# Kernel optimization log

Measured on AMD Instinct MI355X. Metric: run time of the kernel, lower is better.

The kernel has to match this reference:

```python
import jax, jax.numpy as jnp
import numpy as np

D_MODEL = 512
NHEAD = 8
HEAD_DIM = D_MODEL // NHEAD  # 64
ROTARY_DIM = HEAD_DIM        # rotary_dim defaults to head_dim
WINDOW = (127, 128)          # (left, right) sliding window, flash-attn convention
ROPE_BASE = 10000.0


def setup_inputs() -> dict:
    key = jax.random.key(0)
    k1, k2, k3, k4 = jax.random.split(key, 4)
    N, T = 4, 2048
    x = jax.random.normal(k1, (N, T, D_MODEL), dtype=jnp.float32)
    # Wqkv: Linear(d_model, 3*d_model, bias=False) -> weight [3*D, D]
    Wqkv_w = jax.random.normal(k2, (3 * D_MODEL, D_MODEL), dtype=jnp.float32) * (D_MODEL ** -0.5)
    # out_proj: Linear(d_model, d_model, bias=True)
    out_w = jax.random.normal(k3, (D_MODEL, D_MODEL), dtype=jnp.float32) * (D_MODEL ** -0.5)
    out_b = jax.random.normal(k4, (D_MODEL,), dtype=jnp.float32) * 0.01
    return {"x": x, "Wqkv_w": Wqkv_w, "out_w": out_w, "out_b": out_b}


def _rope_cos_sin(T, dtype):
    # flash-attn RotaryEmbedding: inv_freq over even indices of rotary_dim
    inv_freq = 1.0 / (ROPE_BASE ** (jnp.arange(0, ROTARY_DIM, 2, dtype=jnp.float32) / ROTARY_DIM))
    t = jnp.arange(T, dtype=jnp.float32)
    freqs = jnp.outer(t, inv_freq)  # [T, ROTARY_DIM//2]
    return jnp.cos(freqs).astype(dtype), jnp.sin(freqs).astype(dtype)


def _apply_rotary(x, cos, sin):
    # non-interleaved (rotate halves); x: [N, T, H, hd], rotary over first ROTARY_DIM dims
    r, rest = x[..., :ROTARY_DIM], x[..., ROTARY_DIM:]
    half = ROTARY_DIM // 2
    x1, x2 = r[..., :half], r[..., half:]
    c = cos[None, :, None, :]  # [1, T, 1, half]
    s = sin[None, :, None, :]
    rotated = jnp.concatenate([x1 * c - x2 * s, x2 * c + x1 * s], axis=-1)
    return jnp.concatenate([rotated, rest], axis=-1) if rest.shape[-1] else rotated


def reference(x, Wqkv_w, out_w, out_b):
    N, T, D = x.shape
    qkv = jnp.einsum('ntd,ed->nte', x, Wqkv_w).reshape(N, T, 3, NHEAD, HEAD_DIM)
    q, k, v = qkv[:, :, 0], qkv[:, :, 1], qkv[:, :, 2]  # each [N, T, H, hd]
    cos, sin = _rope_cos_sin(T, x.dtype)
    q = _apply_rotary(q, cos, sin)
    k = _apply_rotary(k, cos, sin)
    scale = HEAD_DIM ** -0.5
    scores = jnp.einsum('nthd,nshd->nhts', q, k) * scale  # [N, H, T, T]
    # sliding window: query i attends key j iff i - left <= j <= i + right
    i = jnp.arange(T)[:, None]
    j = jnp.arange(T)[None, :]
    mask = (j >= i - WINDOW[0]) & (j <= i + WINDOW[1])  # [T, T]
    scores = jnp.where(mask[None, None], scores, jnp.finfo(scores.dtype).min)
    attn = jax.nn.softmax(scores, axis=-1)
    ctx = jnp.einsum('nhts,nshd->nthd', attn, v).reshape(N, T, D)
    return jnp.einsum('ntd,ed->nte', ctx, out_w) + out_b
```

## Files before the change

kernel.cpp:

```cpp
#include <hip/hip_runtime.h>
#include <math.h>

#define TSEQ 2048
#define NB 4
#define DM 512
#define NH 8
#define HD 64

typedef _Float16 half8 __attribute__((ext_vector_type(8)));
typedef _Float16 half4 __attribute__((ext_vector_type(4)));
typedef float floatx4 __attribute__((ext_vector_type(4)));

#if __has_builtin(__builtin_amdgcn_exp2f)
#define EXP2F(x) __builtin_amdgcn_exp2f(x)
#else
#define EXP2F(x) exp2f(x)
#endif

__device__ __forceinline__ void gl2lds16(const _Float16* g, _Float16* l) {
  const __attribute__((address_space(1))) unsigned int* gp =
      (const __attribute__((address_space(1))) unsigned int*)(uintptr_t)g;
  __attribute__((address_space(3))) unsigned int* lp =
      (__attribute__((address_space(3))) unsigned int*)(uintptr_t)l;
  __builtin_amdgcn_global_load_lds(gp, lp, 16, 0, 0);
}


__device__ __forceinline__ void cvt8(const float* __restrict__ src, char* __restrict__ dst,
                                     int unit_src, int unit_dst) {
  const float4 a = ((const float4*)src)[2 * unit_src];
  const float4 b = ((const float4*)src)[2 * unit_src + 1];
  half8 h;
  h[0] = (_Float16)a.x; h[1] = (_Float16)a.y; h[2] = (_Float16)a.z; h[3] = (_Float16)a.w;
  h[4] = (_Float16)b.x; h[5] = (_Float16)b.y; h[6] = (_Float16)b.z; h[7] = (_Float16)b.w;
  *(half8*)(dst + (size_t)unit_dst * 16) = h;
}

__global__ void prep(const float* __restrict__ x, const float* __restrict__ wqkv,
                     const float* __restrict__ ow, char* __restrict__ ws) {
  const int i = blockIdx.x * 256 + threadIdx.x;
  if (i < 524288) {
    cvt8(x, ws, i, i);
  } else if (i < 622592) {
    const int o = i - 524288;
    cvt8(wqkv, ws + 8650752, o, o);
  } else if (i < 655360) {
    const int o = i - 622592;
    cvt8(ow, ws + 10485760, o, o);
  } else {
    const int u = i - 655360;
    float4 o4;
    {
      const int id = 2 * u, t = id >> 5, fi = id & 31;
      const float invf = powf(10000.0f, -(float)(2 * fi) * (1.0f / 64.0f));
      float s, c; sincosf((float)t * invf, &s, &c);
      o4.x = c; o4.y = s;
    }
    {
      const int id = 2 * u + 1, t = id >> 5, fi = id & 31;
      const float invf = powf(10000.0f, -(float)(2 * fi) * (1.0f / 64.0f));
      float s, c; sincosf((float)t * invf, &s, &c);
      o4.z = c; o4.w = s;
    }
    ((float4*)(ws + 46137344))[u] = o4;
  }
}

__global__ __launch_bounds__(256) void qkv_gemm_mfma(
    const _Float16* __restrict__ A, const _Float16* __restrict__ B,
    const float2* __restrict__ rope,
    _Float16* __restrict__ qb, _Float16* __restrict__ kb, _Float16* __restrict__ vT)
{
  __shared__ __align__(16) _Float16 As0[128 * 32];
  __shared__ __align__(16) _Float16 Bs0[128 * 32];
  __shared__ __align__(16) _Float16 As1[128 * 32];
  __shared__ __align__(16) _Float16 Bs1[128 * 32];
  const int tid = threadIdx.x;
  const int wv = tid >> 6, lane = tid & 63, quad = lane >> 4, col = lane & 15;
  const int wm = wv >> 1, we = wv & 1;
  const int m0 = blockIdx.x << 7, c0 = blockIdx.y << 7;
  const int r0 = tid >> 2, p0 = tid & 3;
  const int cA0 = (p0 - (r0 >> 1)) & 3;
  const int r1 = (tid + 256) >> 2, p1 = tid & 3;
  const int cA1 = (p1 - (r1 >> 1)) & 3;
  const _Float16* ga0 = &A[(size_t)(m0 + r0) * DM + cA0 * 8];
  const _Float16* ga1 = &A[(size_t)(m0 + r1) * DM + cA1 * 8];
  const _Float16* gb0 = &B[(size_t)(c0 + r0) * DM + cA0 * 8];
  const _Float16* gb1 = &B[(size_t)(c0 + r1) * DM + cA1 * 8];
  floatx4 acc[4][4] = {};

#define QKV_STAGE(AS, BS, K)                      \
  do {                                            \
    gl2lds16(ga0 + (K), &AS[tid * 8]);            \
    gl2lds16(ga1 + (K), &AS[(tid + 256) * 8]);    \
    gl2lds16(gb0 + (K), &BS[tid * 8]);            \
    gl2lds16(gb1 + (K), &BS[(tid + 256) * 8]);    \
  } while (0)

#define QKV_COMPUTE(AS, BS)                                                   \
  do {                                                                        \
    half8 af[4], bf[4];                                                       \
    _Pragma("unroll") for (int mt = 0; mt < 4; mt++) {                        \
      const int R = wm * 64 + mt * 16 + col;                                  \
      af[mt] = *(const half8*)&AS[R * 32 + (((quad + (R >> 1)) & 3) << 3)];   \
    }                                                                         \
    _Pragma("unroll") for (int et = 0; et < 4; et++) {                        \
      const int R = we * 64 + et * 16 + col;                                  \
      bf[et] = *(const half8*)&BS[R * 32 + (((quad + (R >> 1)) & 3) << 3)];   \
    }                                                                         \
    _Pragma("unroll") for (int mt = 0; mt < 4; mt++)                          \
      _Pragma("unroll") for (int et = 0; et < 4; et++)                        \
        acc[mt][et] =                                                         \
            __builtin_amdgcn_mfma_f32_16x16x32_f16(af[mt], bf[et], acc[mt][et], 0, 0, 0); \
  } while (0)

  QKV_STAGE(As0, Bs0, 0);
  for (int k0 = 0; k0 < DM; k0 += 64) {
    __syncthreads();
    QKV_STAGE(As1, Bs1, k0 + 32);
    QKV_COMPUTE(As0, Bs0);
    __syncthreads();
    if (k0 + 64 < DM) QKV_STAGE(As0, Bs0, k0 + 64);
    QKV_COMPUTE(As1, Bs1);
  }
#undef QKV_STAGE
#undef QKV_COMPUTE

  const int eidx = (c0 >> 6) + we;
  const int three = eidx >> 3, h = eidx & 7;
  const int mbase = m0 + wm * 64 + quad * 4;
  if (three == 2) {
#pragma unroll
    for (int mt = 0; mt < 4; mt++) {
      const int m = mbase + mt * 16;
      const int n = m >> 11, t = m & 2047;
#pragma unroll
      for (int et = 0; et < 4; et++) {
        const int dh = et * 16 + col;
        half4 hv;
#pragma unroll
        for (int r = 0; r < 4; r++) hv[r] = (_Float16)acc[mt][et][r];
        *(half4*)&vT[(size_t)(n * NH + h) * HD * TSEQ + (size_t)dh * TSEQ + t] = hv;
      }
    }
  } else {
    _Float16* dst = three ? kb : qb;
    const float scl = three ? 1.0f : 0.125f * 1.4426950408889634f;
#pragma unroll
    for (int mt = 0; mt < 4; mt++)
#pragma unroll
      for (int r = 0; r < 4; r++) {
        const int m = mbase + mt * 16 + r;
        const int n = m >> 11, t = m & 2047;
#pragma unroll
        for (int et = 0; et < 4; et++) {
          const int i = ((et & 1) << 4) + col;
          const float2 cs = rope[t * 32 + i];
          const float v = acc[mt][et][r];
          const float v2 = acc[mt][et ^ 2][r];
          const float o = (et < 2) ? (v * cs.x - v2 * cs.y) : (v * cs.x + v2 * cs.y);
          dst[((size_t)(n * NH + h) * TSEQ + t) * HD + et * 16 + col] = (_Float16)(o * scl);
        }
      }
  }
}

__global__ __launch_bounds__(512, 4) void attn_win_mfma(
    const _Float16* __restrict__ qb, const _Float16* __restrict__ kb,
    const _Float16* __restrict__ vT, _Float16* __restrict__ ctx)
{
  __shared__ __align__(16) char smem[55296];
  _Float16* Ks = (_Float16*)smem;
  _Float16* Vt = (_Float16*)(smem + 9216);
  _Float16* Ps = (_Float16*)(smem + 18432);
  _Float16* Osh = (_Float16*)(smem + 36864);

  const int tid = threadIdx.x;
  const int wv = tid >> 6;
  const int lane = tid & 63;
  const int quad = lane >> 4;
  const int col = lane & 15;
  const int lin = (blockIdx.y << 4) | blockIdx.x;
  const int sl  = ((lin & 7) << 6) | (lin >> 3);
  const int nh = sl >> 4;
  const int q0 = (sl & 15) << 7;
  const _Float16* qp = qb + (size_t)nh * TSEQ * HD;
  const _Float16* kp = kb + (size_t)nh * TSEQ * HD;
  const _Float16* vp = vT + (size_t)nh * HD * TSEQ;

  const int i_row = (wv << 4) + col;
  const int ig = q0 + i_row;
  const half8 qf0 = *(const half8*)&qp[(size_t)ig * HD + (quad << 3)];
  const half8 qf1 = *(const half8*)&qp[(size_t)ig * HD + 32 + (quad << 3)];

  float l_i = 0.0f;
  floatx4 accO[4] = {};

  const int kt0 = max(0, q0 - 127) >> 6;
  const int kt1 = min(TSEQ - 1, q0 + 255) >> 6;
  const int kr = tid >> 3, kc = (tid & 7) << 3;
  const _Float16* kpr = kp + (size_t)kr * HD + kc;
  const _Float16* vpr = vp + (size_t)kr * TSEQ + kc;
  const int iw0 = q0 + (wv << 4);

  half8 ck = *(const half8*)(kpr + (size_t)(kt0 << 6) * HD);
  half8 cv = *(const half8*)(vpr + (kt0 << 6));

  for (int kt = kt0; kt <= kt1; kt++) {
    const int j0 = kt << 6;
    __syncthreads();
    *(half8*)&Ks[kr * 72 + kc] = ck;
    *(half8*)&Vt[kr * 72 + kc] = cv;
    __syncthreads();

    {
      const int jn = (kt < kt1) ? (j0 + 64) : j0;
      ck = *(const half8*)(kpr + (size_t)jn * HD);
      cv = *(const half8*)(vpr + jn);
    }

    if ((unsigned)(j0 - iw0 + 190) >= 334u) continue;

    floatx4 S[4];
#pragma unroll
    for (int js = 0; js < 4; js++) {
      const int jlo = j0 + (js << 4);
      if ((unsigned)(jlo - iw0 + 142) < 286u) {
        const half8 a0 = *(const half8*)&Ks[((js << 4) + col) * 72 + (quad << 3)];
        const half8 a1 = *(const half8*)&Ks[((js << 4) + col) * 72 + 32 + (quad << 3)];
        floatx4 c = {0.f, 0.f, 0.f, 0.f};
        c = __builtin_amdgcn_mfma_f32_16x16x32_f16(a0, qf0, c, 0, 0, 0);
        c = __builtin_amdgcn_mfma_f32_16x16x32_f16(a1, qf1, c, 0, 0, 0);
        S[js] = c;
      }
    }
    const int relb = j0 - ig + 127 + (quad << 2);
#pragma unroll
    for (int js = 0; js < 4; js++) {
      const int jlo = j0 + (js << 4);
      if ((unsigned)(jlo - iw0 + 142) < 286u) {
        half4 ph;
#pragma unroll
        for (int r = 0; r < 4; r++) {
          const bool valid = (unsigned)(relb + (js << 4) + r) < 256u;
          const float p = valid ? EXP2F(S[js][r]) : 0.0f;
          l_i += p;
          ph[r] = (_Float16)p;
        }
        *(half4*)&Ps[i_row * 72 + (js << 4) + (quad << 2)] = ph;
      } else {
        const half4 zz = {(_Float16)0.f, (_Float16)0.f, (_Float16)0.f, (_Float16)0.f};
        *(half4*)&Ps[i_row * 72 + (js << 4) + (quad << 2)] = zz;
      }
    }
    const half8 pa0 = *(const half8*)&Ps[i_row * 72 + (quad << 3)];
    const half8 pa1 = *(const half8*)&Ps[i_row * 72 + 32 + (quad << 3)];
#pragma unroll
    for (int d4 = 0; d4 < 4; d4++) {
      const half8 vb0 = *(const half8*)&Vt[((d4 << 4) + col) * 72 + (quad << 3)];
      const half8 vb1 = *(const half8*)&Vt[((d4 << 4) + col) * 72 + 32 + (quad << 3)];
      accO[d4] = __builtin_amdgcn_mfma_f32_16x16x32_f16(pa0, vb0, accO[d4], 0, 0, 0);
      accO[d4] = __builtin_amdgcn_mfma_f32_16x16x32_f16(pa1, vb1, accO[d4], 0, 0, 0);
    }
  }
  l_i += __shfl_xor(l_i, 16, 64);
  l_i += __shfl_xor(l_i, 32, 64);
  {
    const float linv = 1.0f / l_i;
    float l4[4];
#pragma unroll
    for (int r = 0; r < 4; r++) l4[r] = __shfl(linv, (quad << 2) + r, 64);
#pragma unroll
    for (int d4 = 0; d4 < 4; d4++)
#pragma unroll
      for (int r = 0; r < 4; r++)
        Osh[((wv << 4) + (quad << 2) + r) * 72 + (d4 << 4) + col] = (_Float16)(accO[d4][r] * l4[r]);
  }
  __syncthreads();
  {
    const int n = nh >> 3, h = nh & 7;
    const int oi = tid >> 2, oc = (tid & 3) << 4;
    _Float16* dst = &ctx[((size_t)n * TSEQ + q0 + oi) * DM + h * HD + oc];
    *(half8*)&dst[0] = *(const half8*)&Osh[oi * 72 + oc];
    *(half8*)&dst[8] = *(const half8*)&Osh[oi * 72 + oc + 8];
  }
}

__global__ __launch_bounds__(256) void out_gemm_mfma(
    const _Float16* __restrict__ A, const _Float16* __restrict__ B,
    const float* __restrict__ bias, float* __restrict__ out)
{
  __shared__ __align__(16) _Float16 As0[128 * 32];
  __shared__ __align__(16) _Float16 Bs0[64 * 32];
  __shared__ __align__(16) _Float16 As1[128 * 32];
  __shared__ __align__(16) _Float16 Bs1[64 * 32];
  const int tid = threadIdx.x;
  const int wv = tid >> 6, lane = tid & 63, quad = lane >> 4, col = lane & 15;
  const int wm = wv >> 1, we = wv & 1;
  const int m0 = blockIdx.x << 7, c0 = blockIdx.y << 6;
  const int r0 = tid >> 2, p0 = tid & 3;
  const int cA0 = (p0 - (r0 >> 1)) & 3;
  const int r1 = (tid + 256) >> 2;
  const int cA1 = (p0 - (r1 >> 1)) & 3;
  const _Float16* ga0 = &A[(size_t)(m0 + r0) * DM + cA0 * 8];
  const _Float16* ga1 = &A[(size_t)(m0 + r1) * DM + cA1 * 8];
  const _Float16* gb0 = &B[(size_t)(c0 + r0) * DM + cA0 * 8];
  floatx4 acc[4][2] = {};

#define OG_STAGE(AS, BS, K)                       \
  do {                                            \
    gl2lds16(ga0 + (K), &AS[tid * 8]);            \
    gl2lds16(ga1 + (K), &AS[(tid + 256) * 8]);    \
    gl2lds16(gb0 + (K), &BS[tid * 8]);            \
  } while (0)

#define OG_COMPUTE(AS, BS)                                                    \
  do {                                                                        \
    half8 af[4], bf[2];                                                       \
    _Pragma("unroll") for (int mt = 0; mt < 4; mt++) {                        \
      const int R = wm * 64 + mt * 16 + col;                                  \
      af[mt] = *(const half8*)&AS[R * 32 + (((quad + (R >> 1)) & 3) << 3)];   \
    }                                                                         \
    _Pragma("unroll") for (int et = 0; et < 2; et++) {                        \
      const int R = we * 32 + et * 16 + col;                                  \
      bf[et] = *(const half8*)&BS[R * 32 + (((quad + (R >> 1)) & 3) << 3)];   \
    }                                                                         \
    _Pragma("unroll") for (int mt = 0; mt < 4; mt++)                          \
      _Pragma("unroll") for (int et = 0; et < 2; et++)                        \
        acc[mt][et] =                                                         \
            __builtin_amdgcn_mfma_f32_16x16x32_f16(af[mt], bf[et], acc[mt][et], 0, 0, 0); \
  } while (0)

  OG_STAGE(As0, Bs0, 0);
  for (int k0 = 0; k0 < DM; k0 += 64) {
    __syncthreads();
    OG_STAGE(As1, Bs1, k0 + 32);
    OG_COMPUTE(As0, Bs0);
    __syncthreads();
    if (k0 + 64 < DM) OG_STAGE(As0, Bs0, k0 + 64);
    OG_COMPUTE(As1, Bs1);
  }
#undef OG_STAGE
#undef OG_COMPUTE

  float bb[2];
#pragma unroll
  for (int et = 0; et < 2; et++) bb[et] = bias[c0 + we * 32 + et * 16 + col];
  const int mbase = m0 + wm * 64 + quad * 4;
#pragma unroll
  for (int mt = 0; mt < 4; mt++)
#pragma unroll
    for (int r = 0; r < 4; r++) {
      const int m = mbase + mt * 16 + r;
#pragma unroll
      for (int et = 0; et < 2; et++)
        out[(size_t)m * DM + c0 + we * 32 + et * 16 + col] = acc[mt][et][r] + bb[et];
    }
}

extern "C" void kernel_launch(void* const* d_in, const int* in_sizes, int n_in,
                              void* d_out, int out_size, void* d_ws, size_t ws_size,
                              hipStream_t stream) {
  const float* x    = (const float*)d_in[0];
  const float* wqkv = (const float*)d_in[1];
  const float* ow   = (const float*)d_in[2];
  const float* ob   = (const float*)d_in[3];
  char* ws = (char*)d_ws;
  _Float16* xh    = (_Float16*)(ws);
  _Float16* wqkvh = (_Float16*)(ws + 8650752);
  _Float16* owh   = (_Float16*)(ws + 10485760);
  _Float16* qbuf  = (_Float16*)(ws + 11534336);
  _Float16* kbuf  = (_Float16*)(ws + 20971520);
  _Float16* vTb   = (_Float16*)(ws + 29360128);
  _Float16* ctxh  = (_Float16*)(ws + 37748736);
  float2*   rope  = (float2*)  (ws + 46137344);

  prep<<<2688, 256, 0, stream>>>(x, wqkv, ow, ws);
  qkv_gemm_mfma<<<dim3(64, 12), 256, 0, stream>>>(xh, wqkvh, rope, qbuf, kbuf, vTb);
  attn_win_mfma<<<dim3(16, 32), 512, 0, stream>>>(qbuf, kbuf, vTb, ctxh);
  out_gemm_mfma<<<dim3(64, 8), 256, 0, stream>>>(ctxh, owh, ob, (float*)d_out);
}
```

Baseline: 121.8 us.

## Fuse fp32-to-fp16 conversion of x into QKV GEMM A-tile loads

Result: slower. 146.6 us (+20.4%).

```diff
diff --git a/kernel.cpp b/kernel.cpp
--- a/kernel.cpp
+++ b/kernel.cpp
@@ -36,19 +36,16 @@
   *(half8*)(dst + (size_t)unit_dst * 16) = h;
 }
 
-__global__ void prep(const float* __restrict__ x, const float* __restrict__ wqkv,
+__global__ void prep(const float* __restrict__ wqkv,
                      const float* __restrict__ ow, char* __restrict__ ws) {
   const int i = blockIdx.x * 256 + threadIdx.x;
-  if (i < 524288) {
-    cvt8(x, ws, i, i);
-  } else if (i < 622592) {
-    const int o = i - 524288;
-    cvt8(wqkv, ws + 8650752, o, o);
-  } else if (i < 655360) {
-    const int o = i - 622592;
+  if (i < 98304) {
+    cvt8(wqkv, ws + 8650752, i, i);
+  } else if (i < 131072) {
+    const int o = i - 98304;
     cvt8(ow, ws + 10485760, o, o);
   } else {
-    const int u = i - 655360;
+    const int u = i - 131072;
     float4 o4;
     {
       const int id = 2 * u, t = id >> 5, fi = id & 31;
@@ -67,7 +64,7 @@
 }
 
 __global__ __launch_bounds__(256) void qkv_gemm_mfma(
-    const _Float16* __restrict__ A, const _Float16* __restrict__ B,
+    const float* __restrict__ X, const _Float16* __restrict__ B,
     const float2* __restrict__ rope,
     _Float16* __restrict__ qb, _Float16* __restrict__ kb, _Float16* __restrict__ vT)
 {
@@ -83,18 +80,42 @@
   const int cA0 = (p0 - (r0 >> 1)) & 3;
   const int r1 = (tid + 256) >> 2, p1 = tid & 3;
   const int cA1 = (p1 - (r1 >> 1)) & 3;
-  const _Float16* ga0 = &A[(size_t)(m0 + r0) * DM + cA0 * 8];
-  const _Float16* ga1 = &A[(size_t)(m0 + r1) * DM + cA1 * 8];
+  const float* gx0 = &X[(size_t)(m0 + r0) * DM + cA0 * 8];
+  const float* gx1 = &X[(size_t)(m0 + r1) * DM + cA1 * 8];
   const _Float16* gb0 = &B[(size_t)(c0 + r0) * DM + cA0 * 8];
   const _Float16* gb1 = &B[(size_t)(c0 + r1) * DM + cA1 * 8];
   floatx4 acc[4][4] = {};
-
-#define QKV_STAGE(AS, BS, K)                      \
-  do {                                            \
-    gl2lds16(ga0 + (K), &AS[tid * 8]);            \
-    gl2lds16(ga1 + (K), &AS[(tid + 256) * 8]);    \
-    gl2lds16(gb0 + (K), &BS[tid * 8]);            \
-    gl2lds16(gb1 + (K), &BS[(tid + 256) * 8]);    \
+  float4 fa0, fa1, fa2, fa3;
+
+#define A_LOAD(K)                                    \
+  do {                                               \
+    const float* p0_ = gx0 + (K);                    \
+    const float* p1_ = gx1 + (K);                    \
+    fa0 = *(const float4*)p0_;                       \
+    fa1 = *(const float4*)(p0_ + 4);                 \
+    fa2 = *(const float4*)p1_;                       \
+    fa3 = *(const float4*)(p1_ + 4);                 \
+  } while (0)
+
+#define A_WRITE(AS)                                                        \
+  do {                                                                     \
+    half8 h0_, h1_;                                                        \
+    h0_[0] = (_Float16)fa0.x; h0_[1] = (_Float16)fa0.y;                    \
+    h0_[2] = (_Float16)fa0.z; h0_[3] = (_Float16)fa0.w;                    \
+    h0_[4] = (_Float16)fa1.x; h0_[5] = (_Float16)fa1.y;                    \
+    h0_[6] = (_Float16)fa1.z; h0_[7] = (_Float16)fa1.w;                    \
+    h1_[0] = (_Float16)fa2.x; h1_[1] = (_Float16)fa2.y;                    \
+    h1_[2] = (_Float16)fa2.z; h1_[3] = (_Float16)fa2.w;                    \
+    h1_[4] = (_Float16)fa3.x; h1_[5] = (_Float16)fa3.y;                    \
+    h1_[6] = (_Float16)fa3.z; h1_[7] = (_Float16)fa3.w;                    \
+    *(half8*)&AS[tid * 8] = h0_;                                           \
+    *(half8*)&AS[(tid + 256) * 8] = h1_;                                   \
+  } while (0)
+
+#define B_STAGE(BS, K)                               \
+  do {                                               \
+    gl2lds16(gb0 + (K), &BS[tid * 8]);               \
+    gl2lds16(gb1 + (K), &BS[(tid + 256) * 8]);       \
   } while (0)
 
 #define QKV_COMPUTE(AS, BS)                                                   \
@@ -114,16 +135,27 @@
             __builtin_amdgcn_mfma_f32_16x16x32_f16(af[mt], bf[et], acc[mt][et], 0, 0, 0); \
   } while (0)
 
-  QKV_STAGE(As0, Bs0, 0);
+  A_LOAD(0);
+  A_WRITE(As0);
+  B_STAGE(Bs0, 0);
+  A_LOAD(32);
   for (int k0 = 0; k0 < DM; k0 += 64) {
     __syncthreads();
-    QKV_STAGE(As1, Bs1, k0 + 32);
+    A_WRITE(As1);
+    B_STAGE(Bs1, k0 + 32);
+    A_LOAD(min(k0 + 64, DM - 32));
     QKV_COMPUTE(As0, Bs0);
     __syncthreads();
-    if (k0 + 64 < DM) QKV_STAGE(As0, Bs0, k0 + 64);
+    if (k0 + 64 < DM) {
+      A_WRITE(As0);
+      B_STAGE(Bs0, k0 + 64);
+    }
+    A_LOAD(min(k0 + 96, DM - 32));
     QKV_COMPUTE(As1, Bs1);
   }
-#undef QKV_STAGE
+#undef A_LOAD
+#undef A_WRITE
+#undef B_STAGE
 #undef QKV_COMPUTE
 
   const int eidx = (c0 >> 6) + we;
@@ -366,7 +398,6 @@
   const float* ow   = (const float*)d_in[2];
   const float* ob   = (const float*)d_in[3];
   char* ws = (char*)d_ws;
-  _Float16* xh    = (_Float16*)(ws);
   _Float16* wqkvh = (_Float16*)(ws + 8650752);
   _Float16* owh   = (_Float16*)(ws + 10485760);
   _Float16* qbuf  = (_Float16*)(ws + 11534336);
@@ -375,8 +406,8 @@
   _Float16* ctxh  = (_Float16*)(ws + 37748736);
   float2*   rope  = (float2*)  (ws + 46137344);
 
-  prep<<<2688, 256, 0, stream>>>(x, wqkv, ow, ws);
-  qkv_gemm_mfma<<<dim3(64, 12), 256, 0, stream>>>(xh, wqkvh, rope, qbuf, kbuf, vTb);
+  prep<<<640, 256, 0, stream>>>(wqkv, ow, ws);
+  qkv_gemm_mfma<<<dim3(64, 12), 256, 0, stream>>>(x, wqkvh, rope, qbuf, kbuf, vTb);
   attn_win_mfma<<<dim3(16, 32), 512, 0, stream>>>(qbuf, kbuf, vTb, ctxh);
   out_gemm_mfma<<<dim3(64, 8), 256, 0, stream>>>(ctxh, owh, ob, (float*)d_out);
 }
```
